# Optimization experiments

Measured on AMD Instinct MI355X. Metric: run time of the kernel, lower is better.

The kernel has to match this reference:

```python
import jax, jax.numpy as jnp
import numpy as np

P = 3   # patch_size
D = 7   # displacement window side (odd)
K = 4   # top-k
C = 32  # n_feat
B, H, W = 2, 64, 64
EPS = 1e-12  # F.normalize default eps


def _unfold(x, p):
    """torch F.unfold(x, p, padding=p//2) -> [b, c, p*p, h, w] (row-major patch offsets)."""
    b, c, h, w = x.shape
    pad = p // 2
    xp = jnp.pad(x, ((0, 0), (0, 0), (pad, pad), (pad, pad)))
    return jnp.stack([xp[:, :, i:i + h, j:j + w] for i in range(p) for j in range(p)], axis=2)


def setup_inputs() -> dict:
    key = jax.random.key(0)
    ks = jax.random.split(key, 6)
    feat_t = jax.random.normal(ks[0], (B, C, H, W), jnp.float32)
    feat_tm1 = jax.random.normal(ks[1], (B, C, H, W), jnp.float32)
    # aggregator: Conv2d(k, 1, 1) == weighted sum over k + bias
    agg_w = jax.random.normal(ks[2], (K,), jnp.float32) / K
    agg_b = jax.random.normal(ks[3], (), jnp.float32) * 0.01
    # w_proj: Conv2d(2c, c*p^2, 1) == pointwise linear
    wproj_w = jax.random.normal(ks[4], (C * P * P, 2 * C), jnp.float32) / np.sqrt(2 * C)
    wproj_b = jax.random.normal(ks[5], (C * P * P,), jnp.float32) * 0.01
    return dict(feat_t=feat_t, feat_tm1=feat_tm1, agg_w=agg_w, agg_b=agg_b,
                wproj_w=wproj_w, wproj_b=wproj_b)


def reference(feat_t, feat_tm1, agg_w, agg_b, wproj_w, wproj_b):
    b, c, h, w = feat_t.shape
    p2, d2 = P * P, D * D
    # 3x3 patch unfold of both frames -> [b, c*9, h, w]
    ft_u = _unfold(feat_t, P).reshape(b, c * p2, h, w)
    ftm1_u = _unfold(feat_tm1, P).reshape(b, c * p2, h, w)
    # displacement window over previous-frame patches -> [b, c*9, h, w, d^2]
    disp = jnp.moveaxis(_unfold(ftm1_u, D), 2, -1)
    # cosine similarity along the (c*9) descriptor axis
    ft_n = ft_u / jnp.maximum(jnp.linalg.norm(ft_u, axis=1, keepdims=True), EPS)
    dot = jnp.einsum('bchw,bchwd->bhwd', ft_n, disp)          # [b,h,w,d2]
    dnorm = jnp.maximum(jnp.linalg.norm(disp, axis=1), EPS)    # [b,h,w,d2]
    sim = dot / dnorm
    # top-k displacements per pixel, gather their patch descriptors
    _, idx = jax.lax.top_k(sim, K)                             # [b,h,w,K]
    idx_b = jnp.broadcast_to(idx[:, None], (b, c * p2, h, w, K))
    rel = jnp.take_along_axis(disp, idx_b, axis=-1)            # [b, c*9, h, w, K]
    rel = rel.reshape(b, c, p2, h, w, K)
    # aggregator 1x1 conv over k -> [b, c, h, w, p2]
    agg = jnp.einsum('bcphwk,k->bchwp', rel, agg_w) + agg_b
    # per-pixel patch weights from concatenated features
    cat = jnp.concatenate([feat_t, feat_tm1], axis=1)          # [b, 2c, h, w]
    wgt = jnp.einsum('bihw,oi->bohw', cat, wproj_w) + wproj_b[None, :, None, None]
    wgt = jnp.moveaxis(wgt.reshape(b, c, p2, h, w), 2, -1)     # [b, c, h, w, p2]
    return jnp.sum(agg * wgt, axis=-1)                         # [b, c, h, w]
```

## Files before the change

kernel.cpp:

```cpp
#include <hip/hip_runtime.h>

constexpr float EPSF = 1e-12f;

using short8 = __attribute__((ext_vector_type(8))) short;
using f32x4  = __attribute__((ext_vector_type(4))) float;

__device__ __forceinline__ unsigned short f2bf(float f) {
    unsigned int u = __float_as_uint(f);
    u += 0x7fffu + ((u >> 16) & 1u);
    return (unsigned short)(u >> 16);
}

__global__ __launch_bounds__(512, 4) void agg_mono(
    const float* __restrict__ ft, const float* __restrict__ f1,
    const float* __restrict__ agg_w, const float* __restrict__ agg_bp,
    const float* __restrict__ wproj_w, const float* __restrict__ wproj_b,
    float* __restrict__ out)
{
    __shared__ __align__(16) float pool[16254];
    __shared__ int chosb[16][4];

    float* qw   = pool;
    float* kw   = pool + 1944;
    float* wgtl = pool + 9720;
    float* Tb   = pool + 14904;
    float* Nb   = pool + 15884;
    float* rbnb = pool + 16100;
    unsigned short* Wb = reinterpret_cast<unsigned short*>(pool);
    unsigned short* Bb = reinterpret_cast<unsigned short*>(pool + 14392);

    const int t = threadIdx.x;
    const int pix0 = blockIdx.x << 4;
    const int b  = pix0 >> 12;
    const int y  = (pix0 >> 6) & 63;
    const int x0 = pix0 & 63;

    const float* ftb = ft + ((size_t)b << 17);
    const float* f1b = f1 + ((size_t)b << 17);

    float stgK[14];
    #pragma unroll
    for (int s = 0; s < 14; ++s) {
        int idx = (s << 9) + t;
        if (idx < 6912) {
            int c = idx / 216, rem = idx - c * 216;
            int kr = rem / 24, kc = rem - kr * 24;
            int gy = y - 4 + kr, gx = x0 - 4 + kc;
            stgK[s] = ((unsigned)gy < 64u && (unsigned)gx < 64u)
                    ? f1b[((size_t)c << 12) + (gy << 6) + gx] : 0.f;
        }
    }
    float stgQ[4];
    #pragma unroll
    for (int s = 0; s < 4; ++s) {
        int idx = (s << 9) + t;
        if (idx < 1728) {
            int c = idx / 54, rem = idx - c * 54;
            int qr = rem / 18, qc = rem - qr * 18;
            int gy = y - 1 + qr, gx = x0 - 1 + qc;
            stgQ[s] = ((unsigned)gy < 64u && (unsigned)gx < 64u)
                    ? ftb[((size_t)c << 12) + (gy << 6) + gx] : 0.f;
        }
    }

    #pragma unroll
    for (int s = 0; s < 2; ++s) {
        int idx = (s << 9) + t;
        int i = idx >> 4, ppx = idx & 15;
        const float* src = (i < 32) ? ftb : f1b;
        float v = src[((size_t)(i & 31) << 12) + (y << 6) + x0 + ppx];
        Bb[(((i >> 3) << 4) + ppx) * 8 + (i & 7)] = f2bf(v);
    }

    {
        const float4* w4g = reinterpret_cast<const float4*>(wproj_w);
        #pragma unroll
        for (int s = 0; s < 9; ++s) {
            int f4 = (s << 9) + t;
            float4 wv = w4g[f4];
            int o = f4 >> 4, k4 = f4 & 15;
            int off = ((((o >> 4) << 3) + (k4 >> 1)) * 16 + (o & 15)) * 8
                    + ((k4 & 1) << 2);
            ushort4 bv;
            bv.x = f2bf(wv.x); bv.y = f2bf(wv.y);
            bv.z = f2bf(wv.z); bv.w = f2bf(wv.w);
            *reinterpret_cast<ushort4*>(&Wb[off]) = bv;
        }
    }
    __syncthreads();

    {
        const int lane = t & 63;
        const int wv8 = t >> 6;
        const int lr = lane & 15;
        const int lg = lane >> 4;
        short8 bf0 = *reinterpret_cast<const short8*>(&Bb[(lg * 16 + lr) * 8]);
        short8 bf1 = *reinterpret_cast<const short8*>(&Bb[((4 + lg) * 16 + lr) * 8]);
        #pragma unroll
        for (int ti = 0; ti < 3; ++ti) {
            if (ti == 2 && wv8 >= 2) break;
            const int tt = (ti == 0) ? wv8 : (ti == 1 ? wv8 + 8 : wv8 + 16);
            const float4 bias = *reinterpret_cast<const float4*>(
                wproj_b + tt * 16 + lg * 4);
            f32x4 acc;
            acc[0] = bias.x; acc[1] = bias.y; acc[2] = bias.z; acc[3] = bias.w;
            short8 a0 = *reinterpret_cast<const short8*>(
                &Wb[((tt * 8 + lg) * 16 + lr) * 8]);
            short8 a1 = *reinterpret_cast<const short8*>(
                &Wb[((tt * 8 + 4 + lg) * 16 + lr) * 8]);
            acc = __builtin_amdgcn_mfma_f32_16x16x32_bf16(a0, bf0, acc, 0, 0, 0);
            acc = __builtin_amdgcn_mfma_f32_16x16x32_bf16(a1, bf1, acc, 0, 0, 0);
            *reinterpret_cast<f32x4*>(&wgtl[lr * 292 + tt * 16 + lg * 4]) = acc;
        }
    }
    __syncthreads();

    #pragma unroll
    for (int s = 0; s < 14; ++s) {
        int idx = (s << 9) + t;
        if (idx < 6912) {
            int c = idx / 216, rem = idx - c * 216;
            kw[rem * 36 + c] = stgK[s];
        }
    }
    #pragma unroll
    for (int s = 0; s < 4; ++s) {
        int idx = (s << 9) + t;
        if (idx < 1728) {
            int c = idx / 54, rem = idx - c * 54;
            qw[rem * 36 + c] = stgQ[s];
        }
    }
    __syncthreads();

    if (t < 216) {
        float s = 0.f;
        #pragma unroll
        for (int c4 = 0; c4 < 8; ++c4) {
            float4 v = *reinterpret_cast<const float4*>(&kw[t * 36 + (c4 << 2)]);
            s += v.x * v.x + v.y * v.y + v.z * v.z + v.w * v.w;
        }
        Nb[t] = s;
    }
    __syncthreads();
    if (t < 154) {
        int cyi = t / 22, cxi = t - cyi * 22;
        int kr = cyi + 1, kc = cxi + 1;
        float bn = 0.f;
        #pragma unroll
        for (int di = -1; di <= 1; ++di)
            #pragma unroll
            for (int dj = -1; dj <= 1; ++dj)
                bn += Nb[(kr + di) * 24 + kc + dj];
        rbnb[t] = 1.0f / fmaxf(sqrtf(bn), EPSF);
    }

    {
        const int g = t >> 3, c4 = t & 7;
        #pragma unroll
        for (int pr = 0; pr < 2; ++pr) {
            int p = (pr << 6) + g;
            if (p < 126) {
                int u = p / 18, xx = p - u * 18;
                float av[7] = {0.f, 0.f, 0.f, 0.f, 0.f, 0.f, 0.f};
                #pragma unroll
                for (int r = 0; r < 3; ++r) {
                    float4 qv = *reinterpret_cast<const float4*>(
                        &qw[(r * 18 + xx) * 36 + (c4 << 2)]);
                    #pragma unroll
                    for (int v = 0; v < 7; ++v) {
                        float4 kv = *reinterpret_cast<const float4*>(
                            &kw[((r + u) * 24 + xx + v) * 36 + (c4 << 2)]);
                        av[v] += qv.x * kv.x + qv.y * kv.y + qv.z * kv.z + qv.w * kv.w;
                    }
                }
                #pragma unroll
                for (int v = 0; v < 7; ++v) {
                    float s = av[v];
                    s += __shfl_xor(s, 1, 64);
                    s += __shfl_xor(s, 2, 64);
                    s += __shfl_xor(s, 4, 64);
                    if (c4 == 0) Tb[(u * 7 + v) * 20 + xx] = s;
                }
            }
        }
    }
    __syncthreads();

    {
        const int lane = t & 63;
        const int wvv = t >> 6;
        const int hf = lane >> 5;
        const int c = lane & 31;
        const int ppx = (wvv << 1) + hf;
        float s0 = 0.f, s1;
        {
            int u = c / 7, v = c - u * 7;
            int cy = y + u - 3, cx = x0 + ppx + v - 3;
            if ((unsigned)cy < 64u && (unsigned)cx < 64u) {
                float dot = Tb[c * 20 + ppx] + Tb[c * 20 + ppx + 1]
                          + Tb[c * 20 + ppx + 2];
                s0 = dot * rbnb[u * 22 + ppx + v];
            }
        }
        if (c < 17) {
            int d = c + 32;
            int u = d / 7, v = d - u * 7;
            int cy = y + u - 3, cx = x0 + ppx + v - 3;
            s1 = 0.f;
            if ((unsigned)cy < 64u && (unsigned)cx < 64u) {
                float dot = Tb[d * 20 + ppx] + Tb[d * 20 + ppx + 1]
                          + Tb[d * 20 + ppx + 2];
                s1 = dot * rbnb[u * 22 + ppx + v];
            }
        } else s1 = -3.0e38f;
        #pragma unroll
        for (int k = 0; k < 4; ++k) {
            float bs; int bi;
            if (s0 >= s1) { bs = s0; bi = c; }
            else          { bs = s1; bi = c + 32; }
            #pragma unroll
            for (int off = 16; off; off >>= 1) {
                float os = __shfl_xor(bs, off, 64);
                int   oi = __shfl_xor(bi, off, 64);
                if (os > bs || (os == bs && oi < bi)) { bs = os; bi = oi; }
            }
            if (c == 0) chosb[ppx][k] = bi;
            if (bi == c)           s0 = -3.0e38f;
            else if (bi == c + 32) s1 = -3.0e38f;
        }
    }
    __syncthreads();

    {
        const int px = t & 15;
        const int c  = t >> 4;
        const float ab = agg_bp[0];
        float awv[4];
        #pragma unroll
        for (int k = 0; k < 4; ++k) awv[k] = agg_w[k];
        int uo[4], vo[4]; bool cval[4];
        #pragma unroll
        for (int k = 0; k < 4; ++k) {
            int d = chosb[px][k];
            int u = d / 7, v = d - u * 7;
            int cy = y + u - 3, cx = x0 + px + v - 3;
            cval[k] = ((unsigned)cy < 64u) && ((unsigned)cx < 64u);
            uo[k] = u; vo[k] = v;
        }
        float outv = 0.f;
        #pragma unroll
        for (int j = 0; j < 9; ++j) {
            int pi = j / 3, pj = j - pi * 3;
            float gacc = ab;
            #pragma unroll
            for (int k = 0; k < 4; ++k) {
                float vv = cval[k]
                    ? kw[((uo[k] + pi) * 24 + px + vo[k] + pj) * 36 + c] : 0.f;
                gacc += awv[k] * vv;
            }
            outv += wgtl[px * 292 + c * 9 + j] * gacc;
        }
        out[((size_t)((b << 5) + c) << 12) + (y << 6) + x0 + px] = outv;
    }
}

extern "C" void kernel_launch(void* const* d_in, const int* in_sizes, int n_in,
                              void* d_out, int out_size, void* d_ws, size_t ws_size,
                              hipStream_t stream)
{
    const float* feat_t   = (const float*)d_in[0];
    const float* feat_tm1 = (const float*)d_in[1];
    const float* agg_w    = (const float*)d_in[2];
    const float* agg_b    = (const float*)d_in[3];
    const float* wproj_w  = (const float*)d_in[4];
    const float* wproj_b  = (const float*)d_in[5];
    float* outp = (float*)d_out;
    (void)d_ws; (void)ws_size;

    agg_mono<<<512, 512, 0, stream>>>(feat_t, feat_tm1, agg_w, agg_b,
                                      wproj_w, wproj_b, outp);
}
```

Measured before the change: 22.38 us.

## Halve pixels per block, shrink LDS, load weights directly into MFMA registers

Each block now handles 8 pixels instead of 16, with 384 threads and 1024 blocks, which shrinks the key/query halos and the LDS pool so more blocks can be resident per CU. The projection weights are read from global memory straight into bf16 MFMA operand registers instead of being staged through LDS. The register staging of the halo and one barrier are removed. The cost is a larger relative halo overhead per pixel, redundant weight loads across twice as many blocks, and wasted MFMA columns, since only 8 of the 16 lanes carry valid pixels.

```diff
diff --git a/kernel.cpp b/kernel.cpp
--- a/kernel.cpp
+++ b/kernel.cpp
@@ -11,26 +11,25 @@
     return (unsigned short)(u >> 16);
 }
 
-__global__ __launch_bounds__(512, 4) void agg_mono(
+__global__ __launch_bounds__(384, 6) void agg_mono(
     const float* __restrict__ ft, const float* __restrict__ f1,
     const float* __restrict__ agg_w, const float* __restrict__ agg_bp,
     const float* __restrict__ wproj_w, const float* __restrict__ wproj_b,
     float* __restrict__ out)
 {
-    __shared__ __align__(16) float pool[16254];
-    __shared__ int chosb[16][4];
-
-    float* qw   = pool;
-    float* kw   = pool + 1944;
-    float* wgtl = pool + 9720;
-    float* Tb   = pool + 14904;
-    float* Nb   = pool + 15884;
-    float* rbnb = pool + 16100;
-    unsigned short* Wb = reinterpret_cast<unsigned short*>(pool);
-    unsigned short* Bb = reinterpret_cast<unsigned short*>(pool + 14392);
+    __shared__ __align__(16) float pool[9430];
+    __shared__ int chosb[8][4];
+
+    float* kw   = pool;
+    float* qw   = pool + 5184;
+    float* wgtl = pool + 6264;
+    float* Tb   = pool + 8600;
+    float* Nb   = pool + 9188;
+    float* rbnb = pool + 9332;
+    unsigned short* Bb = reinterpret_cast<unsigned short*>(pool + 8600);
 
     const int t = threadIdx.x;
-    const int pix0 = blockIdx.x << 4;
+    const int pix0 = blockIdx.x << 3;
     const int b  = pix0 >> 12;
     const int y  = (pix0 >> 6) & 63;
     const int x0 = pix0 & 63;
@@ -38,102 +37,78 @@
     const float* ftb = ft + ((size_t)b << 17);
     const float* f1b = f1 + ((size_t)b << 17);
 
-    float stgK[14];
-    #pragma unroll
-    for (int s = 0; s < 14; ++s) {
-        int idx = (s << 9) + t;
-        if (idx < 6912) {
-            int c = idx / 216, rem = idx - c * 216;
-            int kr = rem / 24, kc = rem - kr * 24;
-            int gy = y - 4 + kr, gx = x0 - 4 + kc;
-            stgK[s] = ((unsigned)gy < 64u && (unsigned)gx < 64u)
-                    ? f1b[((size_t)c << 12) + (gy << 6) + gx] : 0.f;
-        }
-    }
-    float stgQ[4];
-    #pragma unroll
-    for (int s = 0; s < 4; ++s) {
-        int idx = (s << 9) + t;
-        if (idx < 1728) {
-            int c = idx / 54, rem = idx - c * 54;
-            int qr = rem / 18, qc = rem - qr * 18;
+    #pragma unroll
+    for (int s = 0; s < 12; ++s) {
+        int idx = s * 384 + t;
+        int c = idx / 144, rem = idx - c * 144;
+        int kr = rem >> 4, kc = rem & 15;
+        int gy = y - 4 + kr, gx = x0 - 4 + kc;
+        float v = ((unsigned)gy < 64u && (unsigned)gx < 64u)
+                ? f1b[((size_t)c << 12) + (gy << 6) + gx] : 0.f;
+        kw[rem * 36 + c] = v;
+    }
+    #pragma unroll
+    for (int s = 0; s < 3; ++s) {
+        int idx = s * 384 + t;
+        if (idx < 960) {
+            int c = idx / 30, rem = idx - c * 30;
+            int qr = rem / 10, qc = rem - qr * 10;
             int gy = y - 1 + qr, gx = x0 - 1 + qc;
-            stgQ[s] = ((unsigned)gy < 64u && (unsigned)gx < 64u)
+            float v = ((unsigned)gy < 64u && (unsigned)gx < 64u)
                     ? ftb[((size_t)c << 12) + (gy << 6) + gx] : 0.f;
-        }
-    }
-
-    #pragma unroll
-    for (int s = 0; s < 2; ++s) {
-        int idx = (s << 9) + t;
-        int i = idx >> 4, ppx = idx & 15;
-        const float* src = (i < 32) ? ftb : f1b;
-        float v = src[((size_t)(i & 31) << 12) + (y << 6) + x0 + ppx];
-        Bb[(((i >> 3) << 4) + ppx) * 8 + (i & 7)] = f2bf(v);
-    }
-
-    {
-        const float4* w4g = reinterpret_cast<const float4*>(wproj_w);
-        #pragma unroll
-        for (int s = 0; s < 9; ++s) {
-            int f4 = (s << 9) + t;
-            float4 wv = w4g[f4];
-            int o = f4 >> 4, k4 = f4 & 15;
-            int off = ((((o >> 4) << 3) + (k4 >> 1)) * 16 + (o & 15)) * 8
-                    + ((k4 & 1) << 2);
-            ushort4 bv;
-            bv.x = f2bf(wv.x); bv.y = f2bf(wv.y);
-            bv.z = f2bf(wv.z); bv.w = f2bf(wv.w);
-            *reinterpret_cast<ushort4*>(&Wb[off]) = bv;
+            qw[rem * 36 + c] = v;
+        }
+    }
+    #pragma unroll
+    for (int s = 0; s < 3; ++s) {
+        int idx = s * 384 + t;
+        if (idx < 1024) {
+            int i = idx >> 4, px16 = idx & 15;
+            float v = 0.f;
+            if (px16 < 8) {
+                const float* src = (i < 32) ? ftb : f1b;
+                v = src[((size_t)(i & 31) << 12) + (y << 6) + x0 + px16];
+            }
+            Bb[(((i >> 3) << 4) + px16) * 8 + (i & 7)] = f2bf(v);
         }
     }
     __syncthreads();
 
     {
         const int lane = t & 63;
-        const int wv8 = t >> 6;
+        const int w6 = t >> 6;
         const int lr = lane & 15;
         const int lg = lane >> 4;
         short8 bf0 = *reinterpret_cast<const short8*>(&Bb[(lg * 16 + lr) * 8]);
         short8 bf1 = *reinterpret_cast<const short8*>(&Bb[((4 + lg) * 16 + lr) * 8]);
         #pragma unroll
         for (int ti = 0; ti < 3; ++ti) {
-            if (ti == 2 && wv8 >= 2) break;
-            const int tt = (ti == 0) ? wv8 : (ti == 1 ? wv8 + 8 : wv8 + 16);
+            const int tt = w6 + 6 * ti;
+            const float* wrow = wproj_w + (size_t)(tt * 16 + lr) * 64 + lg * 8;
+            float4 wa = *reinterpret_cast<const float4*>(wrow);
+            float4 wb = *reinterpret_cast<const float4*>(wrow + 4);
+            float4 wc = *reinterpret_cast<const float4*>(wrow + 32);
+            float4 wd = *reinterpret_cast<const float4*>(wrow + 36);
+            short8 a0, a1;
+            a0[0] = (short)f2bf(wa.x); a0[1] = (short)f2bf(wa.y);
+            a0[2] = (short)f2bf(wa.z); a0[3] = (short)f2bf(wa.w);
+            a0[4] = (short)f2bf(wb.x); a0[5] = (short)f2bf(wb.y);
+            a0[6] = (short)f2bf(wb.z); a0[7] = (short)f2bf(wb.w);
+            a1[0] = (short)f2bf(wc.x); a1[1] = (short)f2bf(wc.y);
+            a1[2] = (short)f2bf(wc.z); a1[3] = (short)f2bf(wc.w);
+            a1[4] = (short)f2bf(wd.x); a1[5] = (short)f2bf(wd.y);
+            a1[6] = (short)f2bf(wd.z); a1[7] = (short)f2bf(wd.w);
             const float4 bias = *reinterpret_cast<const float4*>(
                 wproj_b + tt * 16 + lg * 4);
             f32x4 acc;
             acc[0] = bias.x; acc[1] = bias.y; acc[2] = bias.z; acc[3] = bias.w;
-            short8 a0 = *reinterpret_cast<const short8*>(
-                &Wb[((tt * 8 + lg) * 16 + lr) * 8]);
-            short8 a1 = *reinterpret_cast<const short8*>(
-                &Wb[((tt * 8 + 4 + lg) * 16 + lr) * 8]);
             acc = __builtin_amdgcn_mfma_f32_16x16x32_bf16(a0, bf0, acc, 0, 0, 0);
             acc = __builtin_amdgcn_mfma_f32_16x16x32_bf16(a1, bf1, acc, 0, 0, 0);
-            *reinterpret_cast<f32x4*>(&wgtl[lr * 292 + tt * 16 + lg * 4]) = acc;
-        }
-    }
-    __syncthreads();
-
-    #pragma unroll
-    for (int s = 0; s < 14; ++s) {
-        int idx = (s << 9) + t;
-        if (idx < 6912) {
-            int c = idx / 216, rem = idx - c * 216;
-            kw[rem * 36 + c] = stgK[s];
-        }
-    }
-    #pragma unroll
-    for (int s = 0; s < 4; ++s) {
-        int idx = (s << 9) + t;
-        if (idx < 1728) {
-            int c = idx / 54, rem = idx - c * 54;
-            qw[rem * 36 + c] = stgQ[s];
-        }
-    }
-    __syncthreads();
-
-    if (t < 216) {
+            if (lr < 8)
+                *reinterpret_cast<f32x4*>(&wgtl[lr * 292 + tt * 16 + lg * 4]) = acc;
+        }
+    }
+    if (t < 144) {
         float s = 0.f;
         #pragma unroll
         for (int c4 = 0; c4 < 8; ++c4) {
@@ -143,45 +118,44 @@
         Nb[t] = s;
     }
     __syncthreads();
-    if (t < 154) {
-        int cyi = t / 22, cxi = t - cyi * 22;
-        int kr = cyi + 1, kc = cxi + 1;
+
+    if (t < 98) {
+        int u = t / 14, cxi = t - u * 14;
+        int kr = u + 1, kc = cxi + 1;
         float bn = 0.f;
         #pragma unroll
         for (int di = -1; di <= 1; ++di)
             #pragma unroll
             for (int dj = -1; dj <= 1; ++dj)
-                bn += Nb[(kr + di) * 24 + kc + dj];
+                bn += Nb[(kr + di) * 16 + kc + dj];
         rbnb[t] = 1.0f / fmaxf(sqrtf(bn), EPSF);
     }
 
-    {
-        const int g = t >> 3, c4 = t & 7;
-        #pragma unroll
-        for (int pr = 0; pr < 2; ++pr) {
-            int p = (pr << 6) + g;
-            if (p < 126) {
-                int u = p / 18, xx = p - u * 18;
-                float av[7] = {0.f, 0.f, 0.f, 0.f, 0.f, 0.f, 0.f};
-                #pragma unroll
-                for (int r = 0; r < 3; ++r) {
-                    float4 qv = *reinterpret_cast<const float4*>(
-                        &qw[(r * 18 + xx) * 36 + (c4 << 2)]);
-                    #pragma unroll
-                    for (int v = 0; v < 7; ++v) {
-                        float4 kv = *reinterpret_cast<const float4*>(
-                            &kw[((r + u) * 24 + xx + v) * 36 + (c4 << 2)]);
-                        av[v] += qv.x * kv.x + qv.y * kv.y + qv.z * kv.z + qv.w * kv.w;
-                    }
-                }
+    #pragma unroll
+    for (int s = 0; s < 2; ++s) {
+        int slot = s * 384 + t;
+        if (slot < 560) {
+            int p = slot >> 3, c4 = slot & 7;
+            int u = p / 10, xx = p - u * 10;
+            float av[7] = {0.f, 0.f, 0.f, 0.f, 0.f, 0.f, 0.f};
+            #pragma unroll
+            for (int r = 0; r < 3; ++r) {
+                float4 qv = *reinterpret_cast<const float4*>(
+                    &qw[(r * 10 + xx) * 36 + (c4 << 2)]);
+                const float* kb = &kw[((r + u) * 16 + xx) * 36 + (c4 << 2)];
                 #pragma unroll
                 for (int v = 0; v < 7; ++v) {
-                    float s = av[v];
-                    s += __shfl_xor(s, 1, 64);
-                    s += __shfl_xor(s, 2, 64);
-                    s += __shfl_xor(s, 4, 64);
-                    if (c4 == 0) Tb[(u * 7 + v) * 20 + xx] = s;
-                }
+                    float4 kv = *reinterpret_cast<const float4*>(&kb[v * 36]);
+                    av[v] += qv.x * kv.x + qv.y * kv.y + qv.z * kv.z + qv.w * kv.w;
+                }
+            }
+            #pragma unroll
+            for (int v = 0; v < 7; ++v) {
+                float sv = av[v];
+                sv += __shfl_xor(sv, 1, 64);
+                sv += __shfl_xor(sv, 2, 64);
+                sv += __shfl_xor(sv, 4, 64);
+                if (c4 == 0) Tb[(u * 7 + v) * 12 + xx] = sv;
             }
         }
     }
@@ -189,52 +163,54 @@
 
     {
         const int lane = t & 63;
-        const int wvv = t >> 6;
-        const int hf = lane >> 5;
-        const int c = lane & 31;
-        const int ppx = (wvv << 1) + hf;
-        float s0 = 0.f, s1;
-        {
-            int u = c / 7, v = c - u * 7;
-            int cy = y + u - 3, cx = x0 + ppx + v - 3;
-            if ((unsigned)cy < 64u && (unsigned)cx < 64u) {
-                float dot = Tb[c * 20 + ppx] + Tb[c * 20 + ppx + 1]
-                          + Tb[c * 20 + ppx + 2];
-                s0 = dot * rbnb[u * 22 + ppx + v];
-            }
-        }
-        if (c < 17) {
-            int d = c + 32;
-            int u = d / 7, v = d - u * 7;
-            int cy = y + u - 3, cx = x0 + ppx + v - 3;
-            s1 = 0.f;
-            if ((unsigned)cy < 64u && (unsigned)cx < 64u) {
-                float dot = Tb[d * 20 + ppx] + Tb[d * 20 + ppx + 1]
-                          + Tb[d * 20 + ppx + 2];
-                s1 = dot * rbnb[u * 22 + ppx + v];
-            }
-        } else s1 = -3.0e38f;
-        #pragma unroll
-        for (int k = 0; k < 4; ++k) {
-            float bs; int bi;
-            if (s0 >= s1) { bs = s0; bi = c; }
-            else          { bs = s1; bi = c + 32; }
-            #pragma unroll
-            for (int off = 16; off; off >>= 1) {
-                float os = __shfl_xor(bs, off, 64);
-                int   oi = __shfl_xor(bi, off, 64);
-                if (os > bs || (os == bs && oi < bi)) { bs = os; bi = oi; }
-            }
-            if (c == 0) chosb[ppx][k] = bi;
-            if (bi == c)           s0 = -3.0e38f;
-            else if (bi == c + 32) s1 = -3.0e38f;
-        }
-    }
-    __syncthreads();
-
-    {
-        const int px = t & 15;
-        const int c  = t >> 4;
+        const int w6 = t >> 6;
+        if (w6 < 4) {
+            const int hf = lane >> 5;
+            const int c = lane & 31;
+            const int ppx = (w6 << 1) + hf;
+            float s0 = 0.f, s1;
+            {
+                int u = c / 7, v = c - u * 7;
+                int cy = y + u - 3, cx = x0 + ppx + v - 3;
+                if ((unsigned)cy < 64u && (unsigned)cx < 64u) {
+                    float dot = Tb[c * 12 + ppx] + Tb[c * 12 + ppx + 1]
+                              + Tb[c * 12 + ppx + 2];
+                    s0 = dot * rbnb[u * 14 + ppx + v];
+                }
+            }
+            if (c < 17) {
+                int d = c + 32;
+                int u = d / 7, v = d - u * 7;
+                int cy = y + u - 3, cx = x0 + ppx + v - 3;
+                s1 = 0.f;
+                if ((unsigned)cy < 64u && (unsigned)cx < 64u) {
+                    float dot = Tb[d * 12 + ppx] + Tb[d * 12 + ppx + 1]
+                              + Tb[d * 12 + ppx + 2];
+                    s1 = dot * rbnb[u * 14 + ppx + v];
+                }
+            } else s1 = -3.0e38f;
+            #pragma unroll
+            for (int k = 0; k < 4; ++k) {
+                float bs; int bi;
+                if (s0 >= s1) { bs = s0; bi = c; }
+                else          { bs = s1; bi = c + 32; }
+                #pragma unroll
+                for (int off = 16; off; off >>= 1) {
+                    float os = __shfl_xor(bs, off, 64);
+                    int   oi = __shfl_xor(bi, off, 64);
+                    if (os > bs || (os == bs && oi < bi)) { bs = os; bi = oi; }
+                }
+                if (c == 0) chosb[ppx][k] = bi;
+                if (bi == c)           s0 = -3.0e38f;
+                else if (bi == c + 32) s1 = -3.0e38f;
+            }
+        }
+    }
+    __syncthreads();
+
+    if (t < 256) {
+        const int px = t & 7;
+        const int c  = t >> 3;
         const float ab = agg_bp[0];
         float awv[4];
         #pragma unroll
@@ -256,7 +232,7 @@
             #pragma unroll
             for (int k = 0; k < 4; ++k) {
                 float vv = cval[k]
-                    ? kw[((uo[k] + pi) * 24 + px + vo[k] + pj) * 36 + c] : 0.f;
+                    ? kw[(((uo[k] + pi) << 4) + px + vo[k] + pj) * 36 + c] : 0.f;
                 gacc += awv[k] * vv;
             }
             outv += wgtl[px * 292 + c * 9 + j] * gacc;
@@ -278,6 +254,6 @@
     float* outp = (float*)d_out;
     (void)d_ws; (void)ws_size;
 
-    agg_mono<<<512, 512, 0, stream>>>(feat_t, feat_tm1, agg_w, agg_b,
-                                      wproj_w, wproj_b, outp);
+    agg_mono<<<1024, 384, 0, stream>>>(feat_t, feat_tm1, agg_w, agg_b,
+                                       wproj_w, wproj_b, outp);
 }
```

Result: slower. 47.16 us (+110.8%).

## Load projection weights directly into MFMA registers and drop LDS staging

Applied to the files above, without the earlier changes.

The wproj weights are no longer staged through shared memory. Each wave now reads its rows from global memory, converts them to bf16 and passes them straight to the MFMA. The K/Q windows are written to LDS immediately after loading instead of being held in registers, and one barrier phase plus the register staging arrays are removed. The shared pool shrinks and the launch-bounds occupancy hint is dropped. In exchange, each block does redundant global weight reads and conversions, which should mostly hit in cache, and the kernel gives up the staged overlap between global loads and the MFMA projection.

```diff
diff --git a/kernel.cpp b/kernel.cpp
--- a/kernel.cpp
+++ b/kernel.cpp
@@ -11,22 +11,21 @@
     return (unsigned short)(u >> 16);
 }
 
-__global__ __launch_bounds__(512, 4) void agg_mono(
+__global__ __launch_bounds__(512) void agg_mono(
     const float* __restrict__ ft, const float* __restrict__ f1,
     const float* __restrict__ agg_w, const float* __restrict__ agg_bp,
     const float* __restrict__ wproj_w, const float* __restrict__ wproj_b,
     float* __restrict__ out)
 {
-    __shared__ __align__(16) float pool[16254];
+    __shared__ __align__(16) float pool[15742];
     __shared__ int chosb[16][4];
 
     float* qw   = pool;
     float* kw   = pool + 1944;
     float* wgtl = pool + 9720;
-    float* Tb   = pool + 14904;
-    float* Nb   = pool + 15884;
-    float* rbnb = pool + 16100;
-    unsigned short* Wb = reinterpret_cast<unsigned short*>(pool);
+    float* Tb   = pool + 14392;
+    float* Nb   = pool + 15372;
+    float* rbnb = pool + 15588;
     unsigned short* Bb = reinterpret_cast<unsigned short*>(pool + 14392);
 
     const int t = threadIdx.x;
@@ -38,7 +37,6 @@
     const float* ftb = ft + ((size_t)b << 17);
     const float* f1b = f1 + ((size_t)b << 17);
 
-    float stgK[14];
     #pragma unroll
     for (int s = 0; s < 14; ++s) {
         int idx = (s << 9) + t;
@@ -46,11 +44,11 @@
             int c = idx / 216, rem = idx - c * 216;
             int kr = rem / 24, kc = rem - kr * 24;
             int gy = y - 4 + kr, gx = x0 - 4 + kc;
-            stgK[s] = ((unsigned)gy < 64u && (unsigned)gx < 64u)
+            float v = ((unsigned)gy < 64u && (unsigned)gx < 64u)
                     ? f1b[((size_t)c << 12) + (gy << 6) + gx] : 0.f;
-        }
-    }
-    float stgQ[4];
+            kw[rem * 36 + c] = v;
+        }
+    }
     #pragma unroll
     for (int s = 0; s < 4; ++s) {
         int idx = (s << 9) + t;
@@ -58,34 +56,18 @@
             int c = idx / 54, rem = idx - c * 54;
             int qr = rem / 18, qc = rem - qr * 18;
             int gy = y - 1 + qr, gx = x0 - 1 + qc;
-            stgQ[s] = ((unsigned)gy < 64u && (unsigned)gx < 64u)
+            float v = ((unsigned)gy < 64u && (unsigned)gx < 64u)
                     ? ftb[((size_t)c << 12) + (gy << 6) + gx] : 0.f;
-        }
-    }
-
+            qw[rem * 36 + c] = v;
+        }
+    }
     #pragma unroll
     for (int s = 0; s < 2; ++s) {
         int idx = (s << 9) + t;
-        int i = idx >> 4, ppx = idx & 15;
+        int i = idx >> 4, px16 = idx & 15;
         const float* src = (i < 32) ? ftb : f1b;
-        float v = src[((size_t)(i & 31) << 12) + (y << 6) + x0 + ppx];
-        Bb[(((i >> 3) << 4) + ppx) * 8 + (i & 7)] = f2bf(v);
-    }
-
-    {
-        const float4* w4g = reinterpret_cast<const float4*>(wproj_w);
-        #pragma unroll
-        for (int s = 0; s < 9; ++s) {
-            int f4 = (s << 9) + t;
-            float4 wv = w4g[f4];
-            int o = f4 >> 4, k4 = f4 & 15;
-            int off = ((((o >> 4) << 3) + (k4 >> 1)) * 16 + (o & 15)) * 8
-                    + ((k4 & 1) << 2);
-            ushort4 bv;
-            bv.x = f2bf(wv.x); bv.y = f2bf(wv.y);
-            bv.z = f2bf(wv.z); bv.w = f2bf(wv.w);
-            *reinterpret_cast<ushort4*>(&Wb[off]) = bv;
-        }
+        float v = src[((size_t)(i & 31) << 12) + (y << 6) + x0 + px16];
+        Bb[(((i >> 3) << 4) + px16) * 8 + (i & 7)] = f2bf(v);
     }
     __syncthreads();
 
@@ -100,39 +82,29 @@
         for (int ti = 0; ti < 3; ++ti) {
             if (ti == 2 && wv8 >= 2) break;
             const int tt = (ti == 0) ? wv8 : (ti == 1 ? wv8 + 8 : wv8 + 16);
+            const float* wrow = wproj_w + (size_t)(tt * 16 + lr) * 64 + lg * 8;
+            float4 wa = *reinterpret_cast<const float4*>(wrow);
+            float4 wb = *reinterpret_cast<const float4*>(wrow + 4);
+            float4 wc = *reinterpret_cast<const float4*>(wrow + 32);
+            float4 wd = *reinterpret_cast<const float4*>(wrow + 36);
+            short8 a0, a1;
+            a0[0] = (short)f2bf(wa.x); a0[1] = (short)f2bf(wa.y);
+            a0[2] = (short)f2bf(wa.z); a0[3] = (short)f2bf(wa.w);
+            a0[4] = (short)f2bf(wb.x); a0[5] = (short)f2bf(wb.y);
+            a0[6] = (short)f2bf(wb.z); a0[7] = (short)f2bf(wb.w);
+            a1[0] = (short)f2bf(wc.x); a1[1] = (short)f2bf(wc.y);
+            a1[2] = (short)f2bf(wc.z); a1[3] = (short)f2bf(wc.w);
+            a1[4] = (short)f2bf(wd.x); a1[5] = (short)f2bf(wd.y);
+            a1[6] = (short)f2bf(wd.z); a1[7] = (short)f2bf(wd.w);
             const float4 bias = *reinterpret_cast<const float4*>(
                 wproj_b + tt * 16 + lg * 4);
             f32x4 acc;
             acc[0] = bias.x; acc[1] = bias.y; acc[2] = bias.z; acc[3] = bias.w;
-            short8 a0 = *reinterpret_cast<const short8*>(
-                &Wb[((tt * 8 + lg) * 16 + lr) * 8]);
-            short8 a1 = *reinterpret_cast<const short8*>(
-                &Wb[((tt * 8 + 4 + lg) * 16 + lr) * 8]);
             acc = __builtin_amdgcn_mfma_f32_16x16x32_bf16(a0, bf0, acc, 0, 0, 0);
             acc = __builtin_amdgcn_mfma_f32_16x16x32_bf16(a1, bf1, acc, 0, 0, 0);
             *reinterpret_cast<f32x4*>(&wgtl[lr * 292 + tt * 16 + lg * 4]) = acc;
         }
     }
-    __syncthreads();
-
-    #pragma unroll
-    for (int s = 0; s < 14; ++s) {
-        int idx = (s << 9) + t;
-        if (idx < 6912) {
-            int c = idx / 216, rem = idx - c * 216;
-            kw[rem * 36 + c] = stgK[s];
-        }
-    }
-    #pragma unroll
-    for (int s = 0; s < 4; ++s) {
-        int idx = (s << 9) + t;
-        if (idx < 1728) {
-            int c = idx / 54, rem = idx - c * 54;
-            qw[rem * 36 + c] = stgQ[s];
-        }
-    }
-    __syncthreads();
-
     if (t < 216) {
         float s = 0.f;
         #pragma unroll
@@ -143,6 +115,7 @@
         Nb[t] = s;
     }
     __syncthreads();
+
     if (t < 154) {
         int cyi = t / 22, cxi = t - cyi * 22;
         int kr = cyi + 1, kc = cxi + 1;
@@ -154,7 +127,6 @@
                 bn += Nb[(kr + di) * 24 + kc + dj];
         rbnb[t] = 1.0f / fmaxf(sqrtf(bn), EPSF);
     }
-
     {
         const int g = t >> 3, c4 = t & 7;
         #pragma unroll
```

After: 23.92 us. 6.9% more time.
